# Kernel tuning notes

Measured on AMD Instinct MI355X. Metric: run time of the kernel, lower is better.

## Reference

```python
import jax, jax.numpy as jnp
import numpy as np

H = 32  # rnn/encoder/residual hidden dim
NEG = -1e9


def gru(x, h0, Wih, Whh, bih, bhh):
    # x: (B,T,D), h0: (B,H); torch GRU gate order [r,z,n]
    xp = jnp.swapaxes(x @ Wih.T + bih, 0, 1)  # (T,B,3H)

    def step(h, xt):
        gh = h @ Whh.T + bhh
        xr, xz, xn = jnp.split(xt, 3, axis=-1)
        hr, hz, hn = jnp.split(gh, 3, axis=-1)
        r = jax.nn.sigmoid(xr + hr)
        z = jax.nn.sigmoid(xz + hz)
        n = jnp.tanh(xn + r * hn)
        h_new = (1.0 - z) * n + z * h
        return h_new, h_new

    hT, ys = jax.lax.scan(step, h0, xp)
    return jnp.swapaxes(ys, 0, 1), hT  # (B,T,H), (B,H)


def setup_inputs():
    key = jax.random.key(0)
    ks = jax.random.split(key, 30)
    B, T = 2048, 128
    def lin(k, o, i):
        return jax.random.normal(k, (o, i), jnp.float32) / np.sqrt(i)
    inp = {}
    inp['obs'] = jax.random.normal(ks[0], (B, T, 15), jnp.float32)
    inp['rnn_state'] = jax.random.normal(ks[1], (1, B, 3 * H), jnp.float32)
    inp['enc_air_W'] = lin(ks[2], H, 7); inp['enc_air_b'] = jnp.zeros((H,), jnp.float32)
    inp['enc_m_W'] = lin(ks[3], H, 4); inp['enc_m_b'] = jnp.zeros((H,), jnp.float32)
    inp['air_Wih'] = lin(ks[4], 3 * H, H); inp['air_Whh'] = lin(ks[5], 3 * H, H)
    inp['air_bih'] = jnp.zeros((3 * H,), jnp.float32); inp['air_bhh'] = jnp.zeros((3 * H,), jnp.float32)
    inp['m_Wih'] = lin(ks[6], 3 * H, H); inp['m_Whh'] = lin(ks[7], 3 * H, H)
    inp['m_bih'] = jnp.zeros((3 * H,), jnp.float32); inp['m_bhh'] = jnp.zeros((3 * H,), jnp.float32)
    inp['attn_in_w'] = lin(ks[8], 3 * H, H); inp['attn_in_b'] = jnp.zeros((3 * H,), jnp.float32)
    inp['attn_out_w'] = lin(ks[9], H, H); inp['attn_out_b'] = jnp.zeros((H,), jnp.float32)
    inp['mlp_W0'] = lin(ks[10], 256, 2 * H); inp['mlp_b0'] = jnp.zeros((256,), jnp.float32)
    inp['mlp_W1'] = lin(ks[11], 256, 256); inp['mlp_b1'] = jnp.zeros((256,), jnp.float32)
    inp['out_W'] = lin(ks[12], 1, 256); inp['out_b'] = jnp.zeros((1,), jnp.float32)
    return inp


def reference(obs, rnn_state, enc_air_W, enc_air_b, enc_m_W, enc_m_b,
              air_Wih, air_Whh, air_bih, air_bhh,
              m_Wih, m_Whh, m_bih, m_bhh,
              attn_in_w, attn_in_b, attn_out_w, attn_out_b,
              mlp_W0, mlp_b0, mlp_W1, mlp_b1, out_W, out_b):
    B, T, _ = obs.shape
    h_air0 = rnn_state[0, :, :H]                       # (B,H)
    h_m0 = rnn_state[0, :, H:].reshape(2 * B, H)       # faithful reshape (1,B,64)->(1,2B,32)

    # aircraft branch
    air_emb = obs[..., 8:] @ enc_air_W.T + enc_air_b   # (B,T,H)
    air_feat, next_h_air = gru(air_emb, h_air0, air_Wih, air_Whh, air_bih, air_bhh)

    # missile branch: concat missiles along batch dim
    m_raw = jnp.concatenate([obs[..., 0:4], obs[..., 4:8]], axis=0)  # (2B,T,4)
    m_emb = m_raw @ enc_m_W.T + enc_m_b
    m_feat, next_h_m = gru(m_emb, h_m0, m_Wih, m_Whh, m_bih, m_bhh)
    m1_feat, m2_feat = m_feat[:B], m_feat[B:]

    # inactive-missile mask from raw obs
    obs_flat = obs.reshape(-1, 15)
    inact = jnp.array([1.0, 0.0, 1.0, 0.0], jnp.float32)
    mask = jnp.stack([
        jnp.all(jnp.isclose(obs_flat[:, 0:4], inact), axis=-1),
        jnp.all(jnp.isclose(obs_flat[:, 4:8], inact), axis=-1),
    ], axis=1)                                          # (N,2) True = masked

    N = B * T
    air_flat = air_feat.reshape(N, H)
    m1_flat = m1_feat.reshape(N, H)
    m2_flat = m2_feat.reshape(N, H)

    # 2-head attention, q len 1, kv len 2
    Wq, Wk, Wv = jnp.split(attn_in_w, 3, axis=0)
    bq, bk, bv = jnp.split(attn_in_b, 3, axis=0)
    nh, hd = 2, H // 2
    qh = (air_flat @ Wq.T + bq).reshape(N, nh, hd)
    kv = jnp.stack([m1_flat, m2_flat], axis=1)          # (N,2,H)
    kh = (kv @ Wk.T + bk).reshape(N, 2, nh, hd)
    vh = (kv @ Wv.T + bv).reshape(N, 2, nh, hd)
    scores = jnp.einsum('nhd,nkhd->nhk', qh, kh) / np.sqrt(hd)
    scores = scores + jnp.where(mask[:, None, :], NEG, 0.0)
    w = jax.nn.softmax(scores, axis=-1)
    ctx = jnp.einsum('nhk,nkhd->nhd', w, vh).reshape(N, H)
    attn = ctx @ attn_out_w.T + attn_out_b
    attn = jnp.where(jnp.all(mask, axis=-1, keepdims=True), 0.0, attn)  # torch nan_to_num(all-masked)

    fusion = jnp.concatenate([air_flat, attn], axis=-1)  # (N,2H)
    h1 = jax.nn.leaky_relu(fusion @ mlp_W0.T + mlp_b0, 0.01)
    h2 = jax.nn.leaky_relu(h1 @ mlp_W1.T + mlp_b1, 0.01)
    val = h2 @ out_W.T + out_b                           # (N,1)

    next_h = jnp.concatenate([next_h_air, next_h_m.reshape(B, 2 * H)], axis=-1)[None]  # (1,B,96)
    return val, next_h
```

## Files before the change

### kernel.cpp

```cpp
#include <hip/hip_runtime.h>
#include <hip/hip_bf16.h>

#define BB 2048
#define TT 128
#define NN (BB*TT)
#define NVAL NN

#define OFF_BCA   768u
#define OFF_BCM   1632u
#define OFF_W0P   2048u
#define OFF_W1P   10240u
#define OFF_WQKV  43008u
#define OFF_WO    44544u
#define OFF_WH2A  45568u
#define OFF_WH2M  47104u
#define OFF_WC2A  48640u
#define OFF_WC2M  49024u
#define OFF_AIRF  83968u
#define OFF_MF    8472576u
#define OFF_MASK  25249792u

typedef __attribute__((ext_vector_type(8))) short short8;
typedef __attribute__((ext_vector_type(4))) float f32x4;
typedef _Float16 h2 __attribute__((ext_vector_type(2)));

__device__ __forceinline__ unsigned short f2bf(float f) {
    unsigned u = __builtin_bit_cast(unsigned, f);
    u += 0x7FFFu + ((u >> 16) & 1u);
    return (unsigned short)(u >> 16);
}
__device__ __forceinline__ unsigned f2h(float f) {
    _Float16 h = (_Float16)f;
    return (unsigned)__builtin_bit_cast(unsigned short, h);
}
__device__ __forceinline__ unsigned pkh2(float a, float b) {
    return (f2h(b) << 16) | f2h(a);
}
__device__ __forceinline__ float dot2(unsigned w, unsigned x, float acc) {
    return __builtin_amdgcn_fdot2(__builtin_bit_cast(h2, w),
                                  __builtin_bit_cast(h2, x), acc, false);
}

__global__ __launch_bounds__(256) void prep_kernel(
    const float* __restrict__ enc_air_W, const float* __restrict__ enc_air_b,
    const float* __restrict__ enc_m_W,   const float* __restrict__ enc_m_b,
    const float* __restrict__ air_Wih,   const float* __restrict__ air_bih,
    const float* __restrict__ m_Wih,     const float* __restrict__ m_bih,
    const float* __restrict__ air_Whh,   const float* __restrict__ m_Whh,
    const float* __restrict__ W0,        const float* __restrict__ W1,
    const float* __restrict__ attn_in_w, const float* __restrict__ attn_out_w,
    float* __restrict__ ws)
{
    int b = blockIdx.x, t = threadIdx.x;
    if (b == 0) {
        if (t < 96) {
            float bacc = air_bih[t];
            for (int k = 0; k < 32; k++) bacc += air_Wih[t*32+k] * enc_air_b[k];
            ws[OFF_BCA + t] = bacc;
            float bacc2 = m_bih[t];
            for (int k = 0; k < 32; k++) bacc2 += m_Wih[t*32+k] * enc_m_b[k];
            ws[OFF_BCM + t] = bacc2;
        }
    } else if (b <= 32) {
        unsigned short* w1p = (unsigned short*)(ws + OFF_W1P);
        int base = ((b-1)*256 + t);
        int lane = base & 63;
        int ctf  = base >> 6;
        int ct   = ctf & 15, s = ctf >> 4;
        int col = lane & 15, quad = lane >> 4;
        int k0 = s*32 + quad*8;
        int o  = ct*16 + col;
        #pragma unroll
        for (int j = 0; j < 8; j++)
            w1p[base*8 + j] = f2bf(W1[o*256 + k0 + j]);
    } else if (b <= 40) {
        unsigned short* w0p = (unsigned short*)(ws + OFF_W0P);
        int base = ((b-33)*256 + t);
        int lane = base & 63;
        int ctf  = base >> 6;
        int ct   = ctf & 15, s = ctf >> 4;
        int col = lane & 15, quad = lane >> 4;
        int k0 = s*32 + quad*8;
        int o  = ct*16 + col;
        #pragma unroll
        for (int j = 0; j < 8; j++)
            w0p[base*8 + j] = f2bf(W0[o*64 + k0 + j]);
    } else if (b == 41) {
        unsigned short* wqkv = (unsigned short*)(ws + OFF_WQKV);
        unsigned short* wop  = (unsigned short*)(ws + OFF_WO);
        for (int slot = t; slot < 512; slot += 256) {
            if (slot < 384) {
                int ct = slot >> 6, lane = slot & 63;
                int col = lane & 15, quad = lane >> 4;
                int o = ct*16 + col;
                #pragma unroll
                for (int j = 0; j < 8; j++)
                    wqkv[slot*8 + j] = f2bf(attn_in_w[o*32 + quad*8 + j]);
            } else {
                int s2 = slot - 384;
                int ct = s2 >> 6, lane = s2 & 63;
                int col = lane & 15, quad = lane >> 4;
                #pragma unroll
                for (int j = 0; j < 8; j++)
                    wop[s2*8 + j] = f2bf(attn_out_w[(ct*16+col)*32 + quad*8 + j]);
            }
        }
    } else if (b == 42) {
        unsigned* wa = (unsigned*)(ws + OFF_WH2A);
        unsigned* wm = (unsigned*)(ws + OFF_WH2M);
        for (int s = t; s < 3072; s += 256) {
            int s2 = (s < 1536) ? s : s - 1536;
            const float* W = (s < 1536) ? air_Whh : m_Whh;
            unsigned* dst = (s < 1536) ? wa : wm;
            int o = s2 >> 4, j = s2 & 15;
            dst[s2] = pkh2(W[o*32 + 2*j], W[o*32 + 2*j + 1]);
        }
    } else {
        unsigned* wa = (unsigned*)(ws + OFF_WC2A);
        unsigned* wm = (unsigned*)(ws + OFF_WC2M);
        for (int s = t; s < 768; s += 256) {
            int s2 = (s < 384) ? s : s - 384;
            bool is_air = (s < 384);
            unsigned* dst = is_air ? wa : wm;
            int o = s2 >> 2, j = s2 & 3;
            int ni  = is_air ? 7 : 4;
            float c0 = 0.f, c1 = 0.f;
            int i0 = 2*j, i1 = 2*j + 1;
            if (i0 < ni)
                for (int k = 0; k < 32; k++)
                    c0 += (is_air ? air_Wih[o*32+k]*enc_air_W[k*7+i0]
                                  : m_Wih[o*32+k]*enc_m_W[k*4+i0]);
            if (i1 < ni)
                for (int k = 0; k < 32; k++)
                    c1 += (is_air ? air_Wih[o*32+k]*enc_air_W[k*7+i1]
                                  : m_Wih[o*32+k]*enc_m_W[k*4+i1]);
            dst[s2] = pkh2(c0, c1);
        }
    }
}

template<int NI, int NP, bool DO_MASK>
__device__ void gru_row(const float* __restrict__ in_base,
                        const unsigned* __restrict__ wc2,
                        const float* __restrict__ bc,
                        const unsigned* __restrict__ wh2,
                        const float* __restrict__ bhh,
                        float h0,
                        float* __restrict__ feat_out,
                        float* __restrict__ hT_out,
                        float* __restrict__ mask_out,
                        int lane, int half)
{
    unsigned whr[16], whz[16], whn[16];
    #pragma unroll
    for (int j = 0; j < 16; j++) {
        whr[j] = wh2[lane*16 + j];
        whz[j] = wh2[(32+lane)*16 + j];
        whn[j] = wh2[(64+lane)*16 + j];
    }
    unsigned cr2[NP], cz2[NP], cn2[NP];
    #pragma unroll
    for (int j = 0; j < NP; j++) {
        cr2[j] = wc2[lane*4 + j];
        cz2[j] = wc2[(32+lane)*4 + j];
        cn2[j] = wc2[(64+lane)*4 + j];
    }
    const float bcr = bc[lane], bcz = bc[32+lane], bcn = bc[64+lane];
    const float bhr = bhh[lane], bhz = bhh[32+lane], bhn = bhh[64+lane];

    float h = h0;
    for (int t = 0; t < TT; t++) {
        float xin = (lane < NI) ? in_base[t*15 + lane] : 0.f;

        bool ok = true;
        if (DO_MASK) {
            bool pred = true;
            if (lane < 4) {
                const float c   = ((lane & 1) == 0) ? 1.f : 0.f;
                const float thr = ((lane & 1) == 0) ? 1.00001e-5f : 1e-8f;
                pred = fabsf(xin - c) <= thr;
            }
            unsigned long long ball = __ballot(pred);
            ok = (((ball >> (half*32)) & 0xFull) == 0xFull);
        }

        unsigned x16 = f2h(xin);
        unsigned xnb = (unsigned)__shfl_xor((int)x16, 1, 32);
        unsigned xpk = (xnb << 16) | x16;

        float ar = bcr, az = bcz, an = bcn;
        #pragma unroll
        for (int j = 0; j < NP; j++) {
            unsigned px = (unsigned)__shfl((int)xpk, 2*j, 32);
            ar = dot2(cr2[j], px, ar);
            az = dot2(cz2[j], px, az);
            an = dot2(cn2[j], px, an);
        }

        unsigned h16 = f2h(h);
        unsigned hnb = (unsigned)__shfl_xor((int)h16, 1, 32);
        unsigned hpk = (hnb << 16) | h16;

        float hr = bhr, hz = bhz, hn = bhn;
        #pragma unroll
        for (int j = 0; j < 16; j++) {
            unsigned ph = (unsigned)__shfl((int)hpk, 2*j, 32);
            hr = dot2(whr[j], ph, hr);
            hz = dot2(whz[j], ph, hz);
            hn = dot2(whn[j], ph, hn);
        }

        float r = 1.f / (1.f + __expf(-(ar + hr)));
        float z = 1.f / (1.f + __expf(-(az + hz)));
        float pre = an + r*hn;
        float e2 = __expf(2.f*pre);
        float n = 1.f - 2.f/(e2 + 1.f);
        h = n + z*(h - n);
        feat_out[t*32 + lane] = h;
        if (DO_MASK && lane == 0) mask_out[t*2] = ok ? 1.f : 0.f;
    }
    *hT_out = h;
}

__global__ __launch_bounds__(256) void gru_kernel(
    const float* __restrict__ obs, const float* __restrict__ rnn,
    const float* __restrict__ ws,
    const float* __restrict__ air_bhh, const float* __restrict__ m_bhh,
    float* __restrict__ air_feat, float* __restrict__ m_feat,
    float* __restrict__ mask_f, float* __restrict__ nh_out)
{
    int lane = threadIdx.x & 31;
    int half = (threadIdx.x >> 5) & 1;
    int r = blockIdx.x*8 + (threadIdx.x >> 5);
    if (r < BB) {
        const float* in_base = obs + r*(TT*15) + 8;
        float h0 = rnn[r*96 + lane];
        gru_row<7,4,false>(in_base,
                         (const unsigned*)(ws + OFF_WC2A), ws + OFF_BCA,
                         (const unsigned*)(ws + OFF_WH2A), air_bhh, h0,
                         air_feat + (size_t)r*TT*32,
                         nh_out + r*96 + lane, nullptr, lane, half);
    } else {
        int i = r - BB;
        int b = (i < BB) ? i : i - BB;
        int slot = (i < BB) ? 0 : 1;
        const float* in_base = obs + b*(TT*15) + slot*4;
        float h0 = rnn[(i >> 1)*96 + 32 + (i & 1)*32 + lane];
        gru_row<4,2,true>(in_base,
                        (const unsigned*)(ws + OFF_WC2M), ws + OFF_BCM,
                        (const unsigned*)(ws + OFF_WH2M), m_bhh, h0,
                        m_feat + (size_t)i*TT*32,
                        nh_out + (i >> 1)*96 + 32 + (i & 1)*32 + lane,
                        mask_f + (size_t)(b*TT)*2 + slot, lane, half);
    }
}

__global__ __launch_bounds__(256) void fused_kernel(
    const float* __restrict__ air_feat, const float* __restrict__ m_feat,
    const float* __restrict__ mask_f,
    const unsigned short* __restrict__ wqkv, const float* __restrict__ attn_in_b,
    const unsigned short* __restrict__ wop,  const float* __restrict__ attn_out_b,
    const unsigned short* __restrict__ w0p, const float* __restrict__ b0,
    const unsigned short* __restrict__ w1p, const float* __restrict__ b1,
    const float* __restrict__ outW, const float* __restrict__ outb,
    float* __restrict__ val)
{
    __shared__ unsigned short A1[64*72];
    __shared__ unsigned short U[64*264];
    __shared__ float MS[128];
    __shared__ float PS[4][64];

    unsigned short* AM = U;
    unsigned short* CT = U + 64*72;
    unsigned short* A2 = U;

    const int tid  = threadIdx.x;
    const int lane = tid & 63;
    const int strip = tid >> 6;
    const int col  = lane & 15;
    const int quad = lane >> 4;
    const size_t n0 = (size_t)blockIdx.x * 64;

    {
        const float4* air4 = (const float4*)air_feat;
        const float4* mf4  = (const float4*)m_feat;
        #pragma unroll
        for (int i = 0; i < 2; i++) {
            int f4 = tid + i*256;
            int row = f4 >> 3, c4 = f4 & 7;
            float4 v = air4[(n0+row)*8 + c4];
            ushort4 o; o.x=f2bf(v.x); o.y=f2bf(v.y); o.z=f2bf(v.z); o.w=f2bf(v.w);
            *(ushort4*)&A1[row*72 + c4*4] = o;
        }
        #pragma unroll
        for (int i = 0; i < 2; i++) {
            int f4 = tid + i*256;
            int row = f4 >> 3, c4 = f4 & 7;
            float4 v = mf4[(n0+row)*8 + c4];
            ushort4 o; o.x=f2bf(v.x); o.y=f2bf(v.y); o.z=f2bf(v.z); o.w=f2bf(v.w);
            *(ushort4*)&AM[row*72 + c4*4] = o;
        }
        #pragma unroll
        for (int i = 0; i < 2; i++) {
            int f4 = tid + i*256;
            int row = f4 >> 3, c4 = f4 & 7;
            float4 v = mf4[((size_t)NN + n0 + row)*8 + c4];
            ushort4 o; o.x=f2bf(v.x); o.y=f2bf(v.y); o.z=f2bf(v.z); o.w=f2bf(v.w);
            *(ushort4*)&AM[row*72 + 32 + c4*4] = o;
        }
        if (tid < 128) MS[tid] = mask_f[n0*2 + tid];
    }
    __syncthreads();

    {
        short8 a_air = *(const short8*)&A1[(strip*16 + col)*72 + quad*8];
        short8 a_m1  = *(const short8*)&AM[(strip*16 + col)*72 + quad*8];
        short8 a_m2  = *(const short8*)&AM[(strip*16 + col)*72 + 32 + quad*8];

        f32x4 q[2], k1[2], k2[2], v1[2], v2[2], ao[2];
        #pragma unroll
        for (int ct = 0; ct < 2; ct++) {
            f32x4 z = (f32x4){0.f,0.f,0.f,0.f};
            short8 wqf = *(const short8*)(wqkv + ((0+ct)*64 + lane)*8);
            short8 wkf = *(const short8*)(wqkv + ((2+ct)*64 + lane)*8);
            short8 wvf = *(const short8*)(wqkv + ((4+ct)*64 + lane)*8);
            q[ct]  = __builtin_amdgcn_mfma_f32_16x16x32_bf16(a_air, wqf, z, 0,0,0);
            k1[ct] = __builtin_amdgcn_mfma_f32_16x16x32_bf16(a_m1,  wkf, z, 0,0,0);
            k2[ct] = __builtin_amdgcn_mfma_f32_16x16x32_bf16(a_m2,  wkf, z, 0,0,0);
            v1[ct] = __builtin_amdgcn_mfma_f32_16x16x32_bf16(a_m1,  wvf, z, 0,0,0);
            v2[ct] = __builtin_amdgcn_mfma_f32_16x16x32_bf16(a_m2,  wvf, z, 0,0,0);
        }
        float bqr[2], bkr[2], bvr[2];
        #pragma unroll
        for (int ct = 0; ct < 2; ct++) {
            bqr[ct] = attn_in_b[ct*16 + col];
            bkr[ct] = attn_in_b[32 + ct*16 + col];
            bvr[ct] = attn_in_b[64 + ct*16 + col];
        }
        float p1s[2][4], p2s[2][4];
        #pragma unroll
        for (int ct = 0; ct < 2; ct++) {
            #pragma unroll
            for (int reg = 0; reg < 4; reg++) {
                float qq = q[ct][reg] + bqr[ct];
                float p1 = qq * (k1[ct][reg] + bkr[ct]);
                float p2 = qq * (k2[ct][reg] + bkr[ct]);
                #pragma unroll
                for (int m = 1; m < 16; m <<= 1) {
                    p1 += __shfl_xor(p1, m, 64);
                    p2 += __shfl_xor(p2, m, 64);
                }
                p1s[ct][reg] = p1; p2s[ct][reg] = p2;
            }
        }
        float bothm[4];
        #pragma unroll
        for (int reg = 0; reg < 4; reg++) {
            int rloc = strip*16 + quad*4 + reg;
            float m0v = MS[rloc*2], m1v = MS[rloc*2 + 1];
            bothm[reg] = (m0v > 0.5f && m1v > 0.5f) ? 1.f : 0.f;
            #pragma unroll
            for (int ct = 0; ct < 2; ct++) {
                float s1 = p1s[ct][reg]*0.25f + (m0v > 0.5f ? -1e9f : 0.f);
                float s2 = p2s[ct][reg]*0.25f + (m1v > 0.5f ? -1e9f : 0.f);
                float mx = fmaxf(s1, s2);
                float e1 = __expf(s1 - mx), e2 = __expf(s2 - mx);
                float inv = 1.f/(e1 + e2);
                float ctxv = ((v1[ct][reg] + bvr[ct])*e1 +
                              (v2[ct][reg] + bvr[ct])*e2) * inv;
                CT[rloc*40 + ct*16 + col] = f2bf(ctxv);
            }
        }
        short8 a_ctx = *(const short8*)&CT[(strip*16 + col)*40 + quad*8];
        #pragma unroll
        for (int ct = 0; ct < 2; ct++) {
            f32x4 z = (f32x4){0.f,0.f,0.f,0.f};
            short8 wof = *(const short8*)(wop + (ct*64 + lane)*8);
            ao[ct] = __builtin_amdgcn_mfma_f32_16x16x32_bf16(a_ctx, wof, z, 0,0,0);
        }
        float bor[2] = { attn_out_b[col], attn_out_b[16 + col] };
        #pragma unroll
        for (int reg = 0; reg < 4; reg++) {
            int rloc = strip*16 + quad*4 + reg;
            #pragma unroll
            for (int ct = 0; ct < 2; ct++) {
                float av = ao[ct][reg] + bor[ct];
                av = (bothm[reg] > 0.5f) ? 0.f : av;
                A1[rloc*72 + 32 + ct*16 + col] = f2bf(av);
            }
        }
    }
    __syncthreads();

    float b0r[4], b1r[4], owr[4];
    #pragma unroll
    for (int c = 0; c < 4; c++) {
        int ct = strip*4 + c;
        b0r[c] = b0[ct*16 + col];
        b1r[c] = b1[ct*16 + col];
        owr[c] = outW[ct*16 + col];
    }
    const float outb0 = outb[0];

    f32x4 acc1[4][4];
    #pragma unroll
    for (int s = 0; s < 4; s++)
        #pragma unroll
        for (int c = 0; c < 4; c++) acc1[s][c] = (f32x4){0.f,0.f,0.f,0.f};
    #pragma unroll
    for (int ks = 0; ks < 2; ks++) {
        short8 a[4];
        #pragma unroll
        for (int s = 0; s < 4; s++)
            a[s] = *(const short8*)&A1[(s*16 + col)*72 + ks*32 + quad*8];
        #pragma unroll
        for (int c = 0; c < 4; c++) {
            int ct = strip*4 + c;
            short8 bfr = *(const short8*)(w0p + ((ks*16 + ct)*64 + lane)*8);
            #pragma unroll
            for (int s = 0; s < 4; s++)
                acc1[s][c] = __builtin_amdgcn_mfma_f32_16x16x32_bf16(a[s], bfr, acc1[s][c], 0, 0, 0);
        }
    }
    __syncthreads();
    #pragma unroll
    for (int s = 0; s < 4; s++) {
        #pragma unroll
        for (int c = 0; c < 4; c++) {
            int ct = strip*4 + c;
            #pragma unroll
            for (int reg = 0; reg < 4; reg++) {
                float h = acc1[s][c][reg] + b0r[c];
                h = (h > 0.f) ? h : 0.01f*h;
                A2[(s*16 + quad*4 + reg)*264 + ct*16 + col] = f2bf(h);
            }
        }
    }
    __syncthreads();

    f32x4 acc2[4][4];
    #pragma unroll
    for (int s = 0; s < 4; s++)
        #pragma unroll
        for (int c = 0; c < 4; c++) acc2[s][c] = (f32x4){0.f,0.f,0.f,0.f};
    for (int ks = 0; ks < 8; ks++) {
        short8 a[4];
        #pragma unroll
        for (int s = 0; s < 4; s++)
            a[s] = *(const short8*)&A2[(s*16 + col)*264 + ks*32 + quad*8];
        #pragma unroll
        for (int c = 0; c < 4; c++) {
            int ct = strip*4 + c;
            short8 bfr = *(const short8*)(w1p + ((ks*16 + ct)*64 + lane)*8);
            #pragma unroll
            for (int s = 0; s < 4; s++)
                acc2[s][c] = __builtin_amdgcn_mfma_f32_16x16x32_bf16(a[s], bfr, acc2[s][c], 0, 0, 0);
        }
    }

    #pragma unroll
    for (int s = 0; s < 4; s++) {
        float pv[4];
        #pragma unroll
        for (int reg = 0; reg < 4; reg++) pv[reg] = 0.f;
        #pragma unroll
        for (int c = 0; c < 4; c++) {
            #pragma unroll
            for (int reg = 0; reg < 4; reg++) {
                float h = acc2[s][c][reg] + b1r[c];
                h = (h > 0.f) ? h : 0.01f*h;
                pv[reg] += h*owr[c];
            }
        }
        #pragma unroll
        for (int reg = 0; reg < 4; reg++) {
            #pragma unroll
            for (int m = 1; m < 16; m <<= 1)
                pv[reg] += __shfl_xor(pv[reg], m, 64);
            if (col == 0) PS[strip][s*16 + quad*4 + reg] = pv[reg];
        }
    }
    __syncthreads();
    if (tid < 64)
        val[n0 + tid] = PS[0][tid] + PS[1][tid] + PS[2][tid] + PS[3][tid] + outb0;
}

extern "C" void kernel_launch(void* const* d_in, const int* in_sizes, int n_in,
                              void* d_out, int out_size, void* d_ws, size_t ws_size,
                              hipStream_t stream) {
    const float* obs        = (const float*)d_in[0];
    const float* rnn        = (const float*)d_in[1];
    const float* enc_air_W  = (const float*)d_in[2];
    const float* enc_air_b  = (const float*)d_in[3];
    const float* enc_m_W    = (const float*)d_in[4];
    const float* enc_m_b    = (const float*)d_in[5];
    const float* air_Wih    = (const float*)d_in[6];
    const float* air_Whh    = (const float*)d_in[7];
    const float* air_bih    = (const float*)d_in[8];
    const float* air_bhh    = (const float*)d_in[9];
    const float* m_Wih      = (const float*)d_in[10];
    const float* m_Whh      = (const float*)d_in[11];
    const float* m_bih      = (const float*)d_in[12];
    const float* m_bhh      = (const float*)d_in[13];
    const float* attn_in_w  = (const float*)d_in[14];
    const float* attn_in_b  = (const float*)d_in[15];
    const float* attn_out_w = (const float*)d_in[16];
    const float* attn_out_b = (const float*)d_in[17];
    const float* mlp_W0     = (const float*)d_in[18];
    const float* mlp_b0     = (const float*)d_in[19];
    const float* mlp_W1     = (const float*)d_in[20];
    const float* mlp_b1     = (const float*)d_in[21];
    const float* out_W      = (const float*)d_in[22];
    const float* out_b      = (const float*)d_in[23];

    float* ws  = (float*)d_ws;
    float* out = (float*)d_out;

    prep_kernel<<<44, 256, 0, stream>>>(enc_air_W, enc_air_b, enc_m_W, enc_m_b,
                                        air_Wih, air_bih, m_Wih, m_bih,
                                        air_Whh, m_Whh,
                                        mlp_W0, mlp_W1, attn_in_w, attn_out_w, ws);

    gru_kernel<<<768, 256, 0, stream>>>(obs, rnn, ws, air_bhh, m_bhh,
                                        ws + OFF_AIRF, ws + OFF_MF,
                                        ws + OFF_MASK, out + NVAL);

    fused_kernel<<<NN/64, 256, 0, stream>>>(ws + OFF_AIRF, ws + OFF_MF,
                                            ws + OFF_MASK,
                                            (const unsigned short*)(ws + OFF_WQKV), attn_in_b,
                                            (const unsigned short*)(ws + OFF_WO),   attn_out_b,
                                            (const unsigned short*)(ws + OFF_W0P), mlp_b0,
                                            (const unsigned short*)(ws + OFF_W1P), mlp_b1,
                                            out_W, out_b, out);
}
```

Before: 327.1 us.

## Split MLP hidden layer into two K-halves to cut LDS and registers

The fused MLP now computes the 256-wide first hidden layer in two 128-column halves. Each half is written to a shared buffer half the previous size and immediately consumed as half of the K dimension of the second GEMM. This reduces shared memory per block and the live accumulator registers, and launch bounds now request 4 blocks per SM to raise occupancy. Column-to-strip assignment is interleaved so each half's columns map to all strips. The cost is an extra barrier per half, and register pressure could cause spills.

New measurement: 338.6 us. 3.5% more time.

```diff
diff --git a/kernel.cpp b/kernel.cpp
--- a/kernel.cpp
+++ b/kernel.cpp
@@ -255,7 +255,7 @@
     }
 }
 
-__global__ __launch_bounds__(256) void fused_kernel(
+__global__ __launch_bounds__(256, 4) void fused_kernel(
     const float* __restrict__ air_feat, const float* __restrict__ m_feat,
     const float* __restrict__ mask_f,
     const unsigned short* __restrict__ wqkv, const float* __restrict__ attn_in_b,
@@ -266,13 +266,13 @@
     float* __restrict__ val)
 {
     __shared__ unsigned short A1[64*72];
-    __shared__ unsigned short U[64*264];
+    __shared__ unsigned short U[64*136];
     __shared__ float MS[128];
     __shared__ float PS[4][64];
 
-    unsigned short* AM = U;
-    unsigned short* CT = U + 64*72;
-    unsigned short* A2 = U;
+    unsigned short* AM  = U;
+    unsigned short* CT  = U + 64*72;
+    unsigned short* A2h = U;
 
     const int tid  = threadIdx.x;
     const int lane = tid & 63;
@@ -392,69 +392,76 @@
     }
     __syncthreads();
 
-    float b0r[4], b1r[4], owr[4];
+    float b1r[4], owr[4];
     #pragma unroll
     for (int c = 0; c < 4; c++) {
-        int ct = strip*4 + c;
-        b0r[c] = b0[ct*16 + col];
+        int ct = c*4 + strip;
         b1r[c] = b1[ct*16 + col];
         owr[c] = outW[ct*16 + col];
     }
     const float outb0 = outb[0];
-
-    f32x4 acc1[4][4];
-    #pragma unroll
-    for (int s = 0; s < 4; s++)
-        #pragma unroll
-        for (int c = 0; c < 4; c++) acc1[s][c] = (f32x4){0.f,0.f,0.f,0.f};
-    #pragma unroll
-    for (int ks = 0; ks < 2; ks++) {
-        short8 a[4];
-        #pragma unroll
-        for (int s = 0; s < 4; s++)
-            a[s] = *(const short8*)&A1[(s*16 + col)*72 + ks*32 + quad*8];
-        #pragma unroll
-        for (int c = 0; c < 4; c++) {
-            int ct = strip*4 + c;
-            short8 bfr = *(const short8*)(w0p + ((ks*16 + ct)*64 + lane)*8);
-            #pragma unroll
-            for (int s = 0; s < 4; s++)
-                acc1[s][c] = __builtin_amdgcn_mfma_f32_16x16x32_bf16(a[s], bfr, acc1[s][c], 0, 0, 0);
-        }
-    }
-    __syncthreads();
-    #pragma unroll
-    for (int s = 0; s < 4; s++) {
-        #pragma unroll
-        for (int c = 0; c < 4; c++) {
-            int ct = strip*4 + c;
-            #pragma unroll
-            for (int reg = 0; reg < 4; reg++) {
-                float h = acc1[s][c][reg] + b0r[c];
-                h = (h > 0.f) ? h : 0.01f*h;
-                A2[(s*16 + quad*4 + reg)*264 + ct*16 + col] = f2bf(h);
-            }
-        }
-    }
-    __syncthreads();
 
     f32x4 acc2[4][4];
     #pragma unroll
     for (int s = 0; s < 4; s++)
         #pragma unroll
         for (int c = 0; c < 4; c++) acc2[s][c] = (f32x4){0.f,0.f,0.f,0.f};
-    for (int ks = 0; ks < 8; ks++) {
-        short8 a[4];
-        #pragma unroll
-        for (int s = 0; s < 4; s++)
-            a[s] = *(const short8*)&A2[(s*16 + col)*264 + ks*32 + quad*8];
-        #pragma unroll
-        for (int c = 0; c < 4; c++) {
-            int ct = strip*4 + c;
-            short8 bfr = *(const short8*)(w1p + ((ks*16 + ct)*64 + lane)*8);
+
+    #pragma unroll
+    for (int ch = 0; ch < 2; ch++) {
+        f32x4 acc1[2][4];
+        #pragma unroll
+        for (int cl = 0; cl < 2; cl++)
+            #pragma unroll
+            for (int s = 0; s < 4; s++) acc1[cl][s] = (f32x4){0.f,0.f,0.f,0.f};
+        #pragma unroll
+        for (int ks = 0; ks < 2; ks++) {
+            short8 a[4];
             #pragma unroll
             for (int s = 0; s < 4; s++)
-                acc2[s][c] = __builtin_amdgcn_mfma_f32_16x16x32_bf16(a[s], bfr, acc2[s][c], 0, 0, 0);
+                a[s] = *(const short8*)&A1[(s*16 + col)*72 + ks*32 + quad*8];
+            #pragma unroll
+            for (int cl = 0; cl < 2; cl++) {
+                int ct = (ch*2 + cl)*4 + strip;
+                short8 bfr = *(const short8*)(w0p + ((ks*16 + ct)*64 + lane)*8);
+                #pragma unroll
+                for (int s = 0; s < 4; s++)
+                    acc1[cl][s] = __builtin_amdgcn_mfma_f32_16x16x32_bf16(a[s], bfr, acc1[cl][s], 0, 0, 0);
+            }
+        }
+        if (ch == 1) __syncthreads();
+        #pragma unroll
+        for (int cl = 0; cl < 2; cl++) {
+            int ct = (ch*2 + cl)*4 + strip;
+            float b0v = b0[ct*16 + col];
+            int klocal = (ct - ch*8)*16 + col;
+            #pragma unroll
+            for (int s = 0; s < 4; s++) {
+                #pragma unroll
+                for (int reg = 0; reg < 4; reg++) {
+                    float h = acc1[cl][s][reg] + b0v;
+                    h = (h > 0.f) ? h : 0.01f*h;
+                    A2h[(s*16 + quad*4 + reg)*136 + klocal] = f2bf(h);
+                }
+            }
+        }
+        __syncthreads();
+        #pragma unroll
+        for (int ksl = 0; ksl < 4; ksl++) {
+            int ks = ch*4 + ksl;
+            short8 bfr[4];
+            #pragma unroll
+            for (int c = 0; c < 4; c++) {
+                int ct = c*4 + strip;
+                bfr[c] = *(const short8*)(w1p + ((ks*16 + ct)*64 + lane)*8);
+            }
+            #pragma unroll
+            for (int s = 0; s < 4; s++) {
+                short8 a = *(const short8*)&A2h[(s*16 + col)*136 + ksl*32 + quad*8];
+                #pragma unroll
+                for (int c = 0; c < 4; c++)
+                    acc2[s][c] = __builtin_amdgcn_mfma_f32_16x16x32_bf16(a, bfr[c], acc2[s][c], 0, 0, 0);
+            }
         }
     }
 
```
